# Performance work log

Measured on AMD Instinct MI355X. Metric: run time of the kernel, lower is better.

The kernel has to match this reference:

```python
import jax, jax.numpy as jnp
import numpy as np

IN_C = 256
OUT_C = 256
KS = 3
PAD = 1
EPS = 1e-5
BLOCK_SIZE = 256  # largest power of 2 dividing IN_C
NUM_BLOCKS = IN_C // BLOCK_SIZE


def golay_sequence(n):
    pow2 = 1
    while pow2 < n:
        pow2 *= 2
    a = np.array([1.0], dtype=np.float32)
    b = np.array([1.0], dtype=np.float32)
    while len(a) < pow2:
        a, b = np.concatenate([a, b]), np.concatenate([a, -b])
    return a[:n]


def fwht(x):
    """Unnormalized fast Walsh-Hadamard transform over the last axis (Sylvester order)."""
    base = x.shape[:-1]
    n = x.shape[-1]
    h = 1
    while h < n:
        y = x.reshape(base + (n // (2 * h), 2, h))
        a, c = y[..., 0, :], y[..., 1, :]
        x = jnp.stack([a + c, a - c], axis=-2).reshape(base + (n,))
        h *= 2
    return x


def setup_inputs() -> dict:
    key = jax.random.key(0)
    k1, k2, k3 = jax.random.split(key, 3)
    x = jax.random.normal(k1, (32, IN_C, 56, 56), dtype=jnp.float32)
    fan_in = IN_C * KS * KS
    W = jax.random.normal(k2, (OUT_C, IN_C, KS, KS), dtype=jnp.float32) / np.sqrt(fan_in)
    b = jax.random.normal(k3, (OUT_C,), dtype=jnp.float32) * 0.01
    rms_w = jnp.ones((IN_C,), dtype=jnp.float32)
    return {"x": x, "W": W, "b": b, "rms_w": rms_w}


def reference(x, W, b, rms_w):
    n, c, h, w = x.shape
    golay = jnp.asarray(golay_sequence(c)).reshape(1, c, 1, 1)
    x = x * golay                                    # Golay elementwise multiply
    x = jnp.transpose(x, (0, 2, 3, 1))               # NCHW -> NHWC
    x = x.reshape(n, h, w, NUM_BLOCKS, BLOCK_SIZE)
    x = fwht(x)                                      # blockwise Hadamard butterfly
    x = x.reshape(n, h, w, c)
    # RMSNorm over channel dim
    x = x * jax.lax.rsqrt(jnp.mean(x * x, axis=-1, keepdims=True) + EPS) * rms_w
    x = jnp.transpose(x, (0, 3, 1, 2))               # NHWC -> NCHW
    out = jax.lax.conv_general_dilated(
        x, W, window_strides=(1, 1), padding=((PAD, PAD), (PAD, PAD)),
        dimension_numbers=("NCHW", "OIHW", "NCHW"))
    return out + b[None, :, None, None]
```

## Files before the change

### kernel.cpp

```cpp
#include <hip/hip_runtime.h>
#include <hip/hip_bf16.h>

typedef short v8s __attribute__((ext_vector_type(8)));
typedef float v4f __attribute__((ext_vector_type(4)));
typedef float v16f __attribute__((ext_vector_type(16)));
typedef unsigned short u16;

#define PROW 58
#define PCOL 64

static constexpr size_t A_CC_STRIDE = (size_t)32 * PROW * PCOL * 32;
static constexpr size_t A_BYTES     = 8 * A_CC_STRIDE * 2;
static constexpr size_t WB_ELEMS    = (size_t)9 * 8 * 256 * 32;

__device__ __forceinline__ void gl2lds16(const void* gptr, void* lptr) {
  auto g = (const __attribute__((address_space(1))) unsigned int*)gptr;
  auto l = (__attribute__((address_space(3))) unsigned int*)lptr;
  __builtin_amdgcn_global_load_lds(g, l, 16, 0, 0);
}

__device__ __forceinline__ u16 f2bf(float f) {
  __hip_bfloat16 h = __float2bfloat16(f);
  union { __hip_bfloat16 b; u16 u; } cv; cv.b = h; return cv.u;
}

__global__ __launch_bounds__(256, 2) void fwht_kernel(
    const float* __restrict__ x, const float* __restrict__ rms_w,
    u16* __restrict__ A)
{
  __shared__ __align__(16) char smem[58368];
  float* tile = (float*)smem;
  u16*   ob   = (u16*)smem;

  const int tid = threadIdx.x;
  const int y = blockIdx.x;
  const int n = blockIdx.y;
  const float* src = x + (size_t)n * 256 * 3136 + (size_t)y * 56;
  for (int f = tid; f < 256 * 56; f += 256) {
    int ch = f / 56;
    int xx = f - ch * 56;
    tile[ch * 57 + xx] = src[(size_t)ch * 3136 + xx];
  }
  __syncthreads();

  const int lane = tid & 63;
  const int wv = tid >> 6;
  float gs[4], rw[4];
  #pragma unroll
  for (int k = 0; k < 4; k++) {
    int ch = lane + 64 * k;
    gs[k] = 1.0f - 2.0f * (float)(__popc(ch & (ch >> 1)) & 1);
    rw[k] = rms_w[ch];
  }

  unsigned int res[14][2];
  #pragma unroll
  for (int i = 0; i < 14; i++) {
    const int p = wv + 4 * i;
    float v[4];
    #pragma unroll
    for (int k = 0; k < 4; k++)
      v[k] = tile[(lane + 64 * k) * 57 + p] * gs[k];
    #pragma unroll
    for (int hs = 0; hs < 6; hs++) {
      const int h = 1 << hs;
      #pragma unroll
      for (int k = 0; k < 4; k++) {
        float o = __shfl_xor(v[k], h, 64);
        v[k] = ((lane & h) ? -v[k] : v[k]) + o;
      }
    }
    { float a=v[0], b=v[1], c=v[2], d=v[3];
      v[0]=a+b; v[1]=a-b; v[2]=c+d; v[3]=c-d; }
    { float a=v[0], b=v[1], c=v[2], d=v[3];
      v[0]=a+c; v[2]=a-c; v[1]=b+d; v[3]=b-d; }
    float ss = v[0]*v[0] + v[1]*v[1] + v[2]*v[2] + v[3]*v[3];
    #pragma unroll
    for (int hs = 0; hs < 6; hs++) ss += __shfl_xor(ss, 1 << hs, 64);
    float sc = rsqrtf(ss * (1.0f / 256.0f) + 1e-5f);
    res[i][0] = (unsigned int)f2bf(v[0] * sc * rw[0]) |
                ((unsigned int)f2bf(v[1] * sc * rw[1]) << 16);
    res[i][1] = (unsigned int)f2bf(v[2] * sc * rw[2]) |
                ((unsigned int)f2bf(v[3] * sc * rw[3]) << 16);
  }
  __syncthreads();

  const int icq = (lane >> 3) & 3;
  const int jj = lane & 7;
  const int ccl = lane >> 5;
  #pragma unroll
  for (int i = 0; i < 14; i++) {
    const int p = wv + 4 * i;
    const int sw = ((p + 1) >> 1) & 3;
    const int qs = (icq ^ sw) * 8 + jj;
    #pragma unroll
    for (int k = 0; k < 4; k++) {
      const int cc = 2 * k + ccl;
      u16 val = (u16)(res[i][k >> 1] >> (16 * (k & 1)));
      ob[cc * 1808 + p * 32 + qs] = val;
    }
  }
  __syncthreads();

  const int row = y + 1;
  #pragma unroll
  for (int i = 0; i < 7; i++) {
    int c = tid + 256 * i;
    int cc = c / 224, rem = c - cc * 224;
    v8s val = *(const v8s*)(ob + cc * 1808 + rem * 8);
    size_t go = (((size_t)cc * 32 + n) * PROW + row) * 2048 + 32 + rem * 8;
    *(v8s*)(A + go) = val;
  }
  {
    const v8s z = {0,0,0,0,0,0,0,0};
    int cc = tid >> 5, s = tid & 31;
    size_t rb = (((size_t)cc * 32 + n) * PROW + row) * 2048;
    if (s < 4) *(v8s*)(A + rb + s * 8) = z;
    else       *(v8s*)(A + rb + 57 * 32 + (s - 4) * 8) = z;
  }
  if (y == 0 || y == 55) {
    const v8s z = {0,0,0,0,0,0,0,0};
    const int r = (y == 0) ? 0 : 57;
    #pragma unroll
    for (int i = 0; i < 8; i++) {
      int c = tid + 256 * i;
      int cc = c >> 8, rem = c & 255;
      size_t go = (((size_t)cc * 32 + n) * PROW + r) * 2048 + rem * 8;
      *(v8s*)(A + go) = z;
    }
  }
}

__global__ __launch_bounds__(256) void wconv_kernel(
    const float* __restrict__ Wf, u16* __restrict__ Wb)
{
  int t = blockIdx.x * 256 + threadIdx.x;
  int j = t & 7;
  int icq_st = (t >> 3) & 3;
  int oc = (t >> 5) & 255;
  int cc = (t >> 13) & 7;
  int kk = t >> 16;
  int icq = icq_st ^ ((oc >> 1) & 3);
  int ic = cc * 32 + icq * 8 + j;
  int ky = kk / 3, kx = kk - ky * 3;
  float w = Wf[((oc * 256 + ic) * 3 + ky) * 3 + kx];
  Wb[t] = f2bf(w);
}

__global__ __launch_bounds__(256, 3) void conv_kernel(
    const u16* __restrict__ A, const u16* __restrict__ Wb,
    const float* __restrict__ bias, float* __restrict__ out)
{
  __shared__ __align__(16) u16 As[4 * PCOL * 32];
  __shared__ __align__(16) u16 Bs[3 * 128 * 32];

  const int tid  = threadIdx.x;
  const int lane = tid & 63;
  const int wv   = tid >> 6;
  const int wm   = wv & 1;
  const int wn   = wv >> 1;
  const int m31  = lane & 31;
  const int kh8  = lane >> 5;

  const int ocb = blockIdx.x;
  const int y0  = blockIdx.y * 2;
  const int n   = blockIdx.z;

  const u16* gA = A + ((size_t)n * PROW + y0) * 2048;

  v16f acc[2][2];
  #pragma unroll
  for (int i = 0; i < 2; i++)
    #pragma unroll
    for (int j = 0; j < 2; j++)
      #pragma unroll
      for (int e = 0; e < 16; e++)
        acc[i][j][e] = 0.0f;

  int ub[2][2];
  #pragma unroll
  for (int nf = 0; nf < 2; nf++)
    #pragma unroll
    for (int kh = 0; kh < 2; kh++) {
      int ocl = wn * 64 + nf * 32 + m31;
      int q = kh * 2 + kh8;
      ub[nf][kh] = (ocl * 4 + (q ^ ((ocl >> 1) & 3))) * 8;
    }

  auto stageA = [&](int cc) {
    const u16* g = gA + (size_t)cc * A_CC_STRIDE + tid * 8;
    u16* d = As + tid * 8;
    #pragma unroll
    for (int k = 0; k < 4; k++)
      gl2lds16(g + k * 2048, d + k * 2048);
  };
  auto stageB = [&](int cc, int ky) {
    #pragma unroll
    for (int kx = 0; kx < 3; kx++) {
      const int kk = ky * 3 + kx;
      const u16* g = Wb + ((kk * 8 + cc) * 8192 + ocb * 4096) + tid * 8;
      u16* d = Bs + kx * 4096 + tid * 8;
      gl2lds16(g, d);
      gl2lds16(g + 2048, d + 2048);
    }
  };

  for (int cc = 0; cc < 8; cc++) {
    __syncthreads();
    stageA(cc);
    stageB(cc, 0);
    __syncthreads();
    #pragma unroll
    for (int ky = 0; ky < 3; ky++) {
      #pragma unroll
      for (int kx = 0; kx < 3; kx++) {
        v8s af[2][2];
        #pragma unroll
        for (int mf = 0; mf < 2; mf++)
          #pragma unroll
          for (int kh = 0; kh < 2; kh++) {
            int col = mf * 32 + m31 + kx;
            col = col > 63 ? 63 : col;
            int q = kh * 2 + kh8;
            int ua = (((wm + ky) * PCOL + col) * 4 + (q ^ ((col >> 1) & 3))) * 8;
            af[mf][kh] = *(const v8s*)(As + ua);
          }
        v8s bf[2][2];
        const u16* bsb = Bs + kx * 4096;
        #pragma unroll
        for (int nf = 0; nf < 2; nf++)
          #pragma unroll
          for (int kh = 0; kh < 2; kh++)
            bf[nf][kh] = *(const v8s*)(bsb + ub[nf][kh]);
        #pragma unroll
        for (int mf = 0; mf < 2; mf++)
          #pragma unroll
          for (int nf = 0; nf < 2; nf++) {
            acc[mf][nf] = __builtin_amdgcn_mfma_f32_32x32x16_bf16(af[mf][0], bf[nf][0], acc[mf][nf], 0, 0, 0);
            acc[mf][nf] = __builtin_amdgcn_mfma_f32_32x32x16_bf16(af[mf][1], bf[nf][1], acc[mf][nf], 0, 0, 0);
          }
      }
      if (ky < 2) {
        __syncthreads();
        stageB(cc, ky + 1);
        __syncthreads();
      }
    }
  }

  const int yrow = y0 + wm;
  #pragma unroll
  for (int nf = 0; nf < 2; nf++) {
    const int oc = ocb * 128 + wn * 64 + nf * 32 + m31;
    const float bb = bias[oc];
    float* orow = out + ((size_t)(n * 256 + oc) * 56 + yrow) * 56;
    #pragma unroll
    for (int mf = 0; mf < 2; mf++) {
      #pragma unroll
      for (int g = 0; g < 4; g++) {
        const int x0 = mf * 32 + 8 * g + 4 * kh8;
        if (x0 < 56) {
          v4f val = { acc[mf][nf][4*g+0] + bb, acc[mf][nf][4*g+1] + bb,
                      acc[mf][nf][4*g+2] + bb, acc[mf][nf][4*g+3] + bb };
          *(v4f*)(orow + x0) = val;
        }
      }
    }
  }
}

extern "C" void kernel_launch(void* const* d_in, const int* in_sizes, int n_in,
                              void* d_out, int out_size, void* d_ws, size_t ws_size,
                              hipStream_t stream)
{
  const float* x     = (const float*)d_in[0];
  const float* Wf    = (const float*)d_in[1];
  const float* bias  = (const float*)d_in[2];
  const float* rms_w = (const float*)d_in[3];
  float* out = (float*)d_out;

  if (ws_size < A_BYTES + WB_ELEMS * 2) return;

  u16* Abf = (u16*)d_ws;
  u16* Wb  = (u16*)((char*)d_ws + A_BYTES);

  fwht_kernel<<<dim3(56, 32), 256, 0, stream>>>(x, rms_w, Abf);
  wconv_kernel<<<dim3((int)(WB_ELEMS / 256)), 256, 0, stream>>>(Wf, Wb);
  conv_kernel<<<dim3(2, 28, 32), 256, 0, stream>>>(Abf, Wb, bias, out);
}
```

Measured before the change: 344.7 us.

## Compute Golay-Hadamard transform as bf16 split-precision MFMA matmul in fwht kernel

Replaces the shuffle-based Walsh-Hadamard butterfly with a dense matrix multiply against a precomputed ±1 Hadamard×Golay bf16 table, using MFMA with a hi/lo bf16 split of the input to keep near-fp32 accuracy. The input tile is loaded with direct global-to-LDS async loads, and the output is written straight to global with scalar bf16 stores instead of staging through LDS for vectorized stores. This trades the O(n log n) butterfly and its cross-lane shuffles for O(n^2) matrix-core work plus a 128KB constant table read from global memory. The scattered 2-byte global stores may reduce write efficiency.

Result: no change. 348.1 us (+1.0%).

```diff
diff --git a/kernel.cpp b/kernel.cpp
--- a/kernel.cpp
+++ b/kernel.cpp
@@ -24,97 +24,124 @@
   union { __hip_bfloat16 b; u16 u; } cv; cv.b = h; return cv.u;
 }
 
+struct HgTab {
+  u16 v[16 * 8 * 64 * 8];
+  constexpr HgTab() : v{} {
+    for (int ks = 0; ks < 16; ks++)
+      for (int nt = 0; nt < 8; nt++)
+        for (int l = 0; l < 64; l++)
+          for (int j = 0; j < 8; j++) {
+            int c  = ks * 16 + ((l >> 5) << 3) + j;
+            int cp = (nt << 5) + (l & 31);
+            int s  = (__builtin_popcount((unsigned)(c & cp)) +
+                      __builtin_popcount((unsigned)(c & (c >> 1)))) & 1;
+            v[(((ks << 3) + nt) << 9) + (l << 3) + j] = (u16)(s ? 0xBF80 : 0x3F80);
+          }
+  }
+};
+static_assert(sizeof(HgTab) == 131072, "HgTab size");
+__device__ const HgTab HG{};
+
 __global__ __launch_bounds__(256, 2) void fwht_kernel(
     const float* __restrict__ x, const float* __restrict__ rms_w,
     u16* __restrict__ A)
 {
-  __shared__ __align__(16) char smem[58368];
-  float* tile = (float*)smem;
-  u16*   ob   = (u16*)smem;
+  __shared__ __align__(16) float tile[256 * 56 + 16];
+  __shared__ float ssbuf[2][64];
 
   const int tid = threadIdx.x;
   const int y = blockIdx.x;
   const int n = blockIdx.y;
+
   const float* src = x + (size_t)n * 256 * 3136 + (size_t)y * 56;
-  for (int f = tid; f < 256 * 56; f += 256) {
-    int ch = f / 56;
-    int xx = f - ch * 56;
-    tile[ch * 57 + xx] = src[(size_t)ch * 3136 + xx];
+  #pragma unroll
+  for (int i = 0; i < 14; i++) {
+    int chunk = tid + 256 * i;
+    int c = chunk / 14;
+    int q = chunk - c * 14;
+    gl2lds16(src + (size_t)c * 3136 + q * 4, tile + chunk * 4);
   }
   __syncthreads();
 
   const int lane = tid & 63;
-  const int wv = tid >> 6;
-  float gs[4], rw[4];
-  #pragma unroll
-  for (int k = 0; k < 4; k++) {
-    int ch = lane + 64 * k;
-    gs[k] = 1.0f - 2.0f * (float)(__popc(ch & (ch >> 1)) & 1);
-    rw[k] = rms_w[ch];
-  }
-
-  unsigned int res[14][2];
-  #pragma unroll
-  for (int i = 0; i < 14; i++) {
-    const int p = wv + 4 * i;
-    float v[4];
-    #pragma unroll
-    for (int k = 0; k < 4; k++)
-      v[k] = tile[(lane + 64 * k) * 57 + p] * gs[k];
-    #pragma unroll
-    for (int hs = 0; hs < 6; hs++) {
-      const int h = 1 << hs;
+  const int wv   = tid >> 6;
+  const int mt   = wv & 1;
+  const int nh   = wv >> 1;
+  const int l31  = lane & 31;
+  const int h    = lane >> 5;
+
+  v16f acc[4];
+  #pragma unroll
+  for (int nt = 0; nt < 4; nt++)
+    #pragma unroll
+    for (int e = 0; e < 16; e++)
+      acc[nt][e] = 0.0f;
+
+  const int arow = mt * 32 + l31 + h * (8 * 56);
+
+  #pragma unroll 4
+  for (int ks = 0; ks < 16; ks++) {
+    v8s ah, al;
+    #pragma unroll
+    for (int j = 0; j < 8; j++) {
+      float v = tile[(ks * 16 + j) * 56 + arow];
+      unsigned u  = __float_as_uint(v);
+      unsigned hu = u & 0xFFFF0000u;
+      float r = v - __uint_as_float(hu);
+      ah[j] = (short)(hu >> 16);
+      al[j] = (short)f2bf(r);
+    }
+    #pragma unroll
+    for (int nt = 0; nt < 4; nt++) {
+      v8s b = *(const v8s*)(HG.v + ((size_t)(((ks * 8) + nh * 4 + nt) * 64 + lane)) * 8);
+      acc[nt] = __builtin_amdgcn_mfma_f32_32x32x16_bf16(ah, b, acc[nt], 0, 0, 0);
+      acc[nt] = __builtin_amdgcn_mfma_f32_32x32x16_bf16(al, b, acc[nt], 0, 0, 0);
+    }
+  }
+
+  #pragma unroll
+  for (int g = 0; g < 16; g++) {
+    float s = acc[0][g] * acc[0][g] + acc[1][g] * acc[1][g]
+            + acc[2][g] * acc[2][g] + acc[3][g] * acc[3][g];
+    #pragma unroll
+    for (int m = 1; m <= 16; m <<= 1) s += __shfl_xor(s, m, 64);
+    if (l31 == 0)
+      ssbuf[nh][mt * 32 + (g & 3) + 8 * (g >> 2) + 4 * h] = s;
+  }
+  __syncthreads();
+
+  float rwv[4];
+  #pragma unroll
+  for (int nt = 0; nt < 4; nt++)
+    rwv[nt] = rms_w[nh * 128 + nt * 32 + l31];
+
+  const int jj  = lane & 7;
+  const int icq = l31 >> 3;
+
+  #pragma unroll
+  for (int g = 0; g < 16; g++) {
+    const int rg  = (g & 3) + 8 * (g >> 2) + 4 * h;
+    const int pos = mt * 32 + rg;
+    float ssum = ssbuf[0][pos] + ssbuf[1][pos];
+    float sc = rsqrtf(ssum * (1.0f / 256.0f) + 1e-5f);
+    if (pos < 56) {
+      const int col = pos + 1;
+      const int sw  = (col >> 1) & 3;
+      const int qs  = ((icq ^ sw) << 3) | jj;
+      const size_t rowoff = (size_t)col * 32 + qs;
       #pragma unroll
-      for (int k = 0; k < 4; k++) {
-        float o = __shfl_xor(v[k], h, 64);
-        v[k] = ((lane & h) ? -v[k] : v[k]) + o;
+      for (int nt = 0; nt < 4; nt++) {
+        const int cc = nh * 4 + nt;
+        size_t go = (((size_t)cc * 32 + n) * PROW + (y + 1)) * 2048 + rowoff;
+        A[go] = f2bf(acc[nt][g] * sc * rwv[nt]);
       }
     }
-    { float a=v[0], b=v[1], c=v[2], d=v[3];
-      v[0]=a+b; v[1]=a-b; v[2]=c+d; v[3]=c-d; }
-    { float a=v[0], b=v[1], c=v[2], d=v[3];
-      v[0]=a+c; v[2]=a-c; v[1]=b+d; v[3]=b-d; }
-    float ss = v[0]*v[0] + v[1]*v[1] + v[2]*v[2] + v[3]*v[3];
-    #pragma unroll
-    for (int hs = 0; hs < 6; hs++) ss += __shfl_xor(ss, 1 << hs, 64);
-    float sc = rsqrtf(ss * (1.0f / 256.0f) + 1e-5f);
-    res[i][0] = (unsigned int)f2bf(v[0] * sc * rw[0]) |
-                ((unsigned int)f2bf(v[1] * sc * rw[1]) << 16);
-    res[i][1] = (unsigned int)f2bf(v[2] * sc * rw[2]) |
-                ((unsigned int)f2bf(v[3] * sc * rw[3]) << 16);
-  }
-  __syncthreads();
-
-  const int icq = (lane >> 3) & 3;
-  const int jj = lane & 7;
-  const int ccl = lane >> 5;
-  #pragma unroll
-  for (int i = 0; i < 14; i++) {
-    const int p = wv + 4 * i;
-    const int sw = ((p + 1) >> 1) & 3;
-    const int qs = (icq ^ sw) * 8 + jj;
-    #pragma unroll
-    for (int k = 0; k < 4; k++) {
-      const int cc = 2 * k + ccl;
-      u16 val = (u16)(res[i][k >> 1] >> (16 * (k & 1)));
-      ob[cc * 1808 + p * 32 + qs] = val;
-    }
-  }
-  __syncthreads();
-
-  const int row = y + 1;
-  #pragma unroll
-  for (int i = 0; i < 7; i++) {
-    int c = tid + 256 * i;
-    int cc = c / 224, rem = c - cc * 224;
-    v8s val = *(const v8s*)(ob + cc * 1808 + rem * 8);
-    size_t go = (((size_t)cc * 32 + n) * PROW + row) * 2048 + 32 + rem * 8;
-    *(v8s*)(A + go) = val;
-  }
+  }
+
   {
     const v8s z = {0,0,0,0,0,0,0,0};
     int cc = tid >> 5, s = tid & 31;
-    size_t rb = (((size_t)cc * 32 + n) * PROW + row) * 2048;
+    size_t rb = (((size_t)cc * 32 + n) * PROW + (y + 1)) * 2048;
     if (s < 4) *(v8s*)(A + rb + s * 8) = z;
     else       *(v8s*)(A + rb + 57 * 32 + (s - 4) * 8) = z;
   }
```
